# Kernel tuning notes

Measured on AMD Instinct MI355X. Metric: run time of the kernel, lower is better.

The kernel has to match this reference:

```python
import jax, jax.numpy as jnp
import numpy as np

B, N, F_IN, F_HID, F_OUT = 32, 1024, 512, 512, 512


def setup_inputs() -> dict:
    key = jax.random.key(0)
    ks = jax.random.split(key, 8)
    def xavier(k, fan_in, fan_out):
        bound = float(np.sqrt(6.0 / (fan_in + fan_out)))
        return jax.random.uniform(k, (fan_in, fan_out), jnp.float32, -bound, bound)
    return {
        "batch_graph": jax.random.normal(ks[0], (B, N, F_IN), jnp.float32),
        "adj": jax.random.uniform(ks[1], (B, N, N), jnp.float32),
        "W1": xavier(ks[2], F_IN, F_HID),
        "b1": jnp.zeros((F_HID,), jnp.float32),
        "W2": xavier(ks[3], F_HID, F_HID),
        "b2": jnp.zeros((F_HID,), jnp.float32),
        "W3": xavier(ks[4], F_HID, F_OUT),
        "b3": jnp.zeros((F_OUT,), jnp.float32),
    }


def _gcn_layer(x, adj, W, b):
    # support = X @ W ; out = A @ support + b  (per graph in the batch)
    support = jnp.einsum("bnf,fh->bnh", x, W)
    return jnp.einsum("bnm,bmh->bnh", adj, support) + b


def reference(batch_graph, adj, W1, b1, W2, b2, W3, b3):
    # Block-diagonal big_adj @ big_graph is exactly a batched per-graph matmul:
    # the zero off-diagonal blocks contribute nothing, so math is identical.
    # Dropout is identity at inference (eval mode).
    x = jax.nn.relu(_gcn_layer(batch_graph, adj, W1, b1))
    x = jax.nn.relu(_gcn_layer(x, adj, W2, b2))
    out = _gcn_layer(x, adj, W3, b3)  # [B, N, F_OUT]
    return out
```

## Files before the change

kernel.cpp:

```cpp
#include <hip/hip_runtime.h>
#include <hip/hip_bf16.h>


typedef __attribute__((ext_vector_type(8))) short bf16x8s;
typedef __attribute__((ext_vector_type(4))) float f32x4;
typedef __attribute__((ext_vector_type(4))) unsigned short us4;
typedef __attribute__((ext_vector_type(8))) unsigned short us8;

__device__ __forceinline__ unsigned short f2bf(float f) {
    unsigned u = __builtin_bit_cast(unsigned, f);
    u += 0x7fffu + ((u >> 16) & 1u);
    return (unsigned short)(u >> 16);
}

__device__ __forceinline__ us8 pack8(float4 a, float4 b) {
    us8 o;
    o[0] = f2bf(a.x); o[1] = f2bf(a.y); o[2] = f2bf(a.z); o[3] = f2bf(a.w);
    o[4] = f2bf(b.x); o[5] = f2bf(b.y); o[6] = f2bf(b.z); o[7] = f2bf(b.w);
    return o;
}

__device__ __forceinline__ void async16(const unsigned short* g, unsigned short* l) {
    __builtin_amdgcn_global_load_lds(
        (const __attribute__((address_space(1))) unsigned int*)g,
        (__attribute__((address_space(3))) unsigned int*)l, 16, 0, 0);
}

#define MFMA_(d, va, vb) d = __builtin_amdgcn_mfma_f32_16x16x32_bf16(va, vb, d, 0, 0, 0)

__global__ void prep(const float* __restrict__ W1, const float* __restrict__ W2,
                     const float* __restrict__ W3, unsigned short* __restrict__ WT1,
                     unsigned short* __restrict__ WT2, unsigned short* __restrict__ WT3) {
    constexpr int F = 512;
    const long FF = (long)F * F;
    const long S = (long)gridDim.x * 256;
    for (long k = (long)blockIdx.x * 256 + threadIdx.x; k < 3 * FF; k += S) {
        int w = (int)(k / FF);
        long idx = k % FF;
        int r = (int)(idx % F);
        int c = (int)(idx / F);
        const float* W = (w == 0) ? W1 : (w == 1) ? W2 : W3;
        unsigned short* WT = (w == 0) ? WT1 : (w == 1) ? WT2 : WT3;
        WT[idx] = f2bf(W[(size_t)r * F + c]);
    }
}

__global__ __launch_bounds__(512, 2)
void gemm_g1f(const unsigned short* __restrict__ WT,
              const float* __restrict__ X0,
              unsigned short* __restrict__ PT)
{
    constexpr int K = 512, NN = 1024;
    constexpr int nt = K >> 6;
    __shared__ unsigned short Lraw[65536];

    const int t = threadIdx.x, lane = t & 63, wv = t >> 6;
    const int wm = wv >> 2, wn = wv & 3;
    const int fr = lane & 15, fk = (lane >> 4) * 8, r4 = (lane >> 4) * 4;
    const int lb = ((int)blockIdx.x & 7) * 32 + ((int)blockIdx.x >> 3);
    const int bat = lb >> 3, tt = lb & 7;
    const int m0 = (tt >> 2) << 8, n0 = (tt & 3) << 8;

    const unsigned short* Ab = WT + (size_t)m0 * K;
    const float* Bb = X0 + (size_t)bat * NN * K + (size_t)n0 * K;

    int srow[2], scol[2], lo[2];
#pragma unroll
    for (int r = 0; r < 2; ++r) {
        int c   = r * 512 + t;
        srow[r] = c >> 3;
        scol[r] = ((c & 7) * 8) ^ ((srow[r] & 7) << 3);
        lo[r]   = c * 8;
    }

    auto stageA = [&](int kt, int h) {
        unsigned short* base = Lraw + (kt & 1) * 16384;
#pragma unroll
        for (int r = 0; r < 2; ++r)
            async16(Ab + (size_t)(h * 128 + srow[r]) * K + kt * 64 + scol[r],
                    base + h * 8192 + lo[r]);
    };
    auto rdA = [&](int buf, int mf, int kkj) -> bf16x8s {
        int row = wm * 128 + mf * 16 + fr;
        int e   = (kkj * 32 + fk) ^ ((row & 7) << 3);
        return *(const bf16x8s*)&Lraw[buf * 16384 + row * 64 + e];
    };
    auto rdB = [&](int buf, int nf, int kkj) -> bf16x8s {
        int row = wn * 64 + nf * 16 + fr;
        int e   = (kkj * 32 + fk) ^ ((row & 7) << 3);
        return *(const bf16x8s*)&Lraw[32768 + buf * 16384 + row * 64 + e];
    };

    float4 fa[4], fb[4];
    auto loadB = [&](int kt) {
#pragma unroll
        for (int h = 0; h < 2; ++h)
#pragma unroll
            for (int r = 0; r < 2; ++r) {
                const float* p = Bb + (size_t)(h * 128 + srow[r]) * K + kt * 64 + scol[r];
                fa[h * 2 + r] = *(const float4*)p;
                fb[h * 2 + r] = *(const float4*)(p + 4);
            }
    };
    auto writeB = [&](int buf) {
#pragma unroll
        for (int h = 0; h < 2; ++h)
#pragma unroll
            for (int r = 0; r < 2; ++r)
                *(us8*)&Lraw[32768 + buf * 16384 + h * 8192 + lo[r]] =
                    pack8(fa[h * 2 + r], fb[h * 2 + r]);
    };

    f32x4 acc[8][4];
#pragma unroll
    for (int i = 0; i < 8; ++i)
#pragma unroll
        for (int j = 0; j < 4; ++j) acc[i][j] = f32x4{0.f, 0.f, 0.f, 0.f};
    bf16x8s aP[4], aB[4], aC[4], bX[4], bY[4];

    loadB(0);
    stageA(0, 0); stageA(0, 1);
    writeB(0);
    loadB(1);
    asm volatile("s_waitcnt vmcnt(8)" ::: "memory");
    __syncthreads();
#pragma unroll
    for (int m = 0; m < 4; ++m) aP[m] = rdA(0, m, 0);
#pragma unroll
    for (int n = 0; n < 4; ++n) bX[n] = rdB(0, n, 0);

    for (int it = 0; it < nt; ++it) {
        const int cur = it & 1, nxt = cur ^ 1;
        const bool m1 = it + 1 < nt, m2 = it + 2 < nt;

        __builtin_amdgcn_s_barrier();
#pragma unroll
        for (int m = 0; m < 4; ++m) aB[m] = rdA(cur, m + 4, 0);
        if (m1) { stageA(it + 1, 0); stageA(it + 1, 1); }
        __builtin_amdgcn_s_setprio(1);
#pragma unroll
        for (int m = 0; m < 4; ++m)
#pragma unroll
            for (int n = 0; n < 4; ++n) MFMA_(acc[m][n], aP[m], bX[n]);
        __builtin_amdgcn_s_setprio(0);

        __builtin_amdgcn_s_barrier();
#pragma unroll
        for (int m = 0; m < 4; ++m) aC[m] = rdA(cur, m, 1);
#pragma unroll
        for (int n = 0; n < 4; ++n) bY[n] = rdB(cur, n, 1);
        __builtin_amdgcn_s_setprio(1);
#pragma unroll
        for (int m = 0; m < 4; ++m)
#pragma unroll
            for (int n = 0; n < 4; ++n) MFMA_(acc[m + 4][n], aB[m], bX[n]);
        __builtin_amdgcn_s_setprio(0);

        __builtin_amdgcn_s_barrier();
#pragma unroll
        for (int m = 0; m < 4; ++m) aB[m] = rdA(cur, m + 4, 1);
        if (m1) writeB(nxt);
        if (m2) loadB(it + 2);
        __builtin_amdgcn_s_setprio(1);
#pragma unroll
        for (int m = 0; m < 4; ++m)
#pragma unroll
            for (int n = 0; n < 4; ++n) MFMA_(acc[m][n], aC[m], bY[n]);
        __builtin_amdgcn_s_setprio(0);

        if (m1) {
            if (m2) asm volatile("s_waitcnt vmcnt(8) lgkmcnt(0)" ::: "memory");
            else    asm volatile("s_waitcnt vmcnt(0) lgkmcnt(0)" ::: "memory");
            __builtin_amdgcn_s_barrier();
#pragma unroll
            for (int m = 0; m < 4; ++m) aP[m] = rdA(nxt, m, 0);
#pragma unroll
            for (int n = 0; n < 4; ++n) bX[n] = rdB(nxt, n, 0);
        }
        __builtin_amdgcn_s_setprio(1);
#pragma unroll
        for (int m = 0; m < 4; ++m)
#pragma unroll
            for (int n = 0; n < 4; ++n) MFMA_(acc[m + 4][n], aB[m], bY[n]);
        __builtin_amdgcn_s_setprio(0);
    }

    __syncthreads();
    const int R0 = m0 + wm * 128;
    const int C0 = n0 + wn * 64;
    unsigned short* sl = Lraw + wv * 8192;
#pragma unroll
    for (int i = 0; i < 8; ++i)
#pragma unroll
        for (int j = 0; j < 4; ++j)
#pragma unroll
            for (int e = 0; e < 4; ++e) {
                const int row = i * 16 + r4 + e;
                const int col = j * 16 + fr;
                sl[row * 64 + (col ^ ((row & 7) << 3))] = f2bf(acc[i][j][e]);
            }
    unsigned short* Cb = PT + (size_t)bat * 512 * 1024;
#pragma unroll
    for (int rr = 0; rr < 16; ++rr) {
        const int row = rr * 8 + (lane >> 3);
        const int k8  = lane & 7;
        us8 v = *(const us8*)&sl[row * 64 + ((k8 ^ (row & 7)) << 3)];
        *(us8*)&Cb[(size_t)(R0 + row) * NN + C0 + k8 * 8] = v;
    }
}

__global__ __launch_bounds__(512, 2)
void gemm_g2f(const float* __restrict__ ADJ,
              unsigned short* __restrict__ adjb,
              const unsigned short* __restrict__ PT,
              unsigned short* __restrict__ P1,
              const float* __restrict__ bias)
{
    constexpr int K = 1024, NN = 512;
    constexpr int nt = K >> 6;
    __shared__ unsigned short Lraw[81920];

    const int t = threadIdx.x, lane = t & 63, wv = t >> 6;
    const int wm = wv >> 2, wn = wv & 3;
    const int fr = lane & 15, fk = (lane >> 4) * 8, r4 = (lane >> 4) * 4;
    const int lb = ((int)blockIdx.x & 7) * 32 + ((int)blockIdx.x >> 3);
    const int bat = lb >> 3, tt = lb & 7;
    const int m0 = (tt >> 1) << 8, n0 = (tt & 1) << 8;
    const bool wb = (n0 == 0);

    const float* Afb = ADJ + (size_t)bat * K * K + (size_t)m0 * K;
    unsigned short* Awb = adjb + (size_t)bat * K * K + (size_t)m0 * K;
    const unsigned short* Bb = PT + (size_t)bat * NN * K + (size_t)n0 * K;

    int srow[2], scol[2], lo[2];
#pragma unroll
    for (int r = 0; r < 2; ++r) {
        int c   = r * 512 + t;
        srow[r] = c >> 3;
        scol[r] = ((c & 7) * 8) ^ ((srow[r] & 7) << 3);
        lo[r]   = c * 8;
    }

    auto stageB = [&](int buf, int kt) {
        unsigned short* base = Lraw + 32768 + buf * 16384;
#pragma unroll
        for (int h = 0; h < 2; ++h)
#pragma unroll
            for (int r = 0; r < 2; ++r)
                async16(Bb + (size_t)(h * 128 + srow[r]) * K + kt * 64 + scol[r],
                        base + h * 8192 + lo[r]);
    };
    auto rdA = [&](int buf, int mf, int kkj) -> bf16x8s {
        int row = wm * 128 + mf * 16 + fr;
        int e   = (kkj * 32 + fk) ^ ((row & 7) << 3);
        return *(const bf16x8s*)&Lraw[buf * 16384 + row * 64 + e];
    };
    auto rdB = [&](int buf, int nf, int kkj) -> bf16x8s {
        int row = wn * 64 + nf * 16 + fr;
        int e   = (kkj * 32 + fk) ^ ((row & 7) << 3);
        return *(const bf16x8s*)&Lraw[32768 + buf * 16384 + row * 64 + e];
    };

    float4 fa[4], fb[4];
    auto loadA = [&](int kt) {
#pragma unroll
        for (int h = 0; h < 2; ++h)
#pragma unroll
            for (int r = 0; r < 2; ++r) {
                const float* p = Afb + (size_t)(h * 128 + srow[r]) * K + kt * 64 + scol[r];
                fa[h * 2 + r] = *(const float4*)p;
                fb[h * 2 + r] = *(const float4*)(p + 4);
            }
    };
    auto flushA = [&](int buf, int kt) {
#pragma unroll
        for (int h = 0; h < 2; ++h)
#pragma unroll
            for (int r = 0; r < 2; ++r) {
                us8 v = pack8(fa[h * 2 + r], fb[h * 2 + r]);
                *(us8*)&Lraw[buf * 16384 + h * 8192 + lo[r]] = v;
                if (wb)
                    *(us8*)&Awb[(size_t)(h * 128 + srow[r]) * K + kt * 64 + scol[r]] = v;
            }
    };

    f32x4 acc[8][4];
#pragma unroll
    for (int i = 0; i < 8; ++i)
#pragma unroll
        for (int j = 0; j < 4; ++j) acc[i][j] = f32x4{0.f, 0.f, 0.f, 0.f};
    bf16x8s aP[4], aB[4], aC[4], bX[4], bY[4];

    loadA(0);
    stageB(0, 0); stageB(1, 1);
    flushA(0, 0);
    loadA(1);
    asm volatile("s_waitcnt vmcnt(4)" ::: "memory");
    __syncthreads();
#pragma unroll
    for (int m = 0; m < 4; ++m) aP[m] = rdA(0, m, 0);
#pragma unroll
    for (int n = 0; n < 4; ++n) bX[n] = rdB(0, n, 0);

    int bc = 0;
    for (int it = 0; it < nt; ++it) {
        const int cur = it & 1, nxt = cur ^ 1;
        const int bn1 = (bc == 2) ? 0 : bc + 1;
        const int bn2 = (bn1 == 2) ? 0 : bn1 + 1;
        const bool m1 = it + 1 < nt, m2 = it + 2 < nt;

        __builtin_amdgcn_s_barrier();
#pragma unroll
        for (int m = 0; m < 4; ++m) aB[m] = rdA(cur, m + 4, 0);
        __builtin_amdgcn_s_setprio(1);
#pragma unroll
        for (int m = 0; m < 4; ++m)
#pragma unroll
            for (int n = 0; n < 4; ++n) MFMA_(acc[m][n], aP[m], bX[n]);
        __builtin_amdgcn_s_setprio(0);

        __builtin_amdgcn_s_barrier();
#pragma unroll
        for (int m = 0; m < 4; ++m) aC[m] = rdA(cur, m, 1);
#pragma unroll
        for (int n = 0; n < 4; ++n) bY[n] = rdB(bc, n, 1);
        __builtin_amdgcn_s_setprio(1);
#pragma unroll
        for (int m = 0; m < 4; ++m)
#pragma unroll
            for (int n = 0; n < 4; ++n) MFMA_(acc[m + 4][n], aB[m], bX[n]);
        __builtin_amdgcn_s_setprio(0);

        __builtin_amdgcn_s_barrier();
#pragma unroll
        for (int m = 0; m < 4; ++m) aB[m] = rdA(cur, m + 4, 1);
        if (m1) flushA(nxt, it + 1);
        if (m2) stageB(bn2, it + 2);
        __builtin_amdgcn_s_setprio(1);
#pragma unroll
        for (int m = 0; m < 4; ++m)
#pragma unroll
            for (int n = 0; n < 4; ++n) MFMA_(acc[m][n], aC[m], bY[n]);
        __builtin_amdgcn_s_setprio(0);

        if (m1) {
            if (m2) asm volatile("s_waitcnt vmcnt(12) lgkmcnt(0)" ::: "memory");
            else    asm volatile("s_waitcnt vmcnt(0) lgkmcnt(0)" ::: "memory");
            __builtin_amdgcn_s_barrier();
#pragma unroll
            for (int m = 0; m < 4; ++m) aP[m] = rdA(nxt, m, 0);
#pragma unroll
            for (int n = 0; n < 4; ++n) bX[n] = rdB(bn1, n, 0);
            if (m2) loadA(it + 2);
        }
        __builtin_amdgcn_s_setprio(1);
#pragma unroll
        for (int m = 0; m < 4; ++m)
#pragma unroll
            for (int n = 0; n < 4; ++n) MFMA_(acc[m + 4][n], aB[m], bY[n]);
        __builtin_amdgcn_s_setprio(0);
        bc = bn1;
    }

    __syncthreads();
    const int R0 = m0 + wm * 128;
    const int C0 = n0 + wn * 64;
    float bv[4];
#pragma unroll
    for (int j = 0; j < 4; ++j) bv[j] = bias[C0 + j * 16 + fr];
    unsigned short* sl = Lraw + wv * 8192;
#pragma unroll
    for (int i = 0; i < 8; ++i)
#pragma unroll
        for (int j = 0; j < 4; ++j)
#pragma unroll
            for (int e = 0; e < 4; ++e) {
                const int row = i * 16 + r4 + e;
                const int col = j * 16 + fr;
                sl[row * 64 + (col ^ ((row & 7) << 3))] =
                    f2bf(fmaxf(acc[i][j][e] + bv[j], 0.f));
            }
    unsigned short* Cb = P1 + (size_t)bat * 1024 * 512;
#pragma unroll
    for (int rr = 0; rr < 16; ++rr) {
        const int row = rr * 8 + (lane >> 3);
        const int k8  = lane & 7;
        us8 v = *(const us8*)&sl[row * 64 + ((k8 ^ (row & 7)) << 3)];
        *(us8*)&Cb[(size_t)(R0 + row) * NN + C0 + k8 * 8] = v;
    }
}

template<bool RELU, bool OUT_F32>
__global__ __launch_bounds__(512, 2)
void gemm256(const unsigned short* __restrict__ A,
             const unsigned short* __restrict__ BT,
             void* __restrict__ Cout,
             const float* __restrict__ bias,
             int M, int N, int K,
             long sA, long sBT, long sC)
{
    __shared__ unsigned short Lraw[81920];

    const int t    = threadIdx.x;
    const int lane = t & 63;
    const int wv   = t >> 6;
    const int wm   = wv >> 2;
    const int wn   = wv & 3;
    const int fr   = lane & 15;
    const int fk   = (lane >> 4) * 8;
    const int r4   = (lane >> 4) * 4;

    const int tilesN = N >> 8;
    const int bpb    = (M >> 8) * tilesN;
    const int cpx = gridDim.x >> 3;
    const int lb  = (blockIdx.x & 7) * cpx + (blockIdx.x >> 3);
    const int bat = lb / bpb;
    const int tt  = lb % bpb;
    const int m0  = (tt / tilesN) << 8;
    const int n0  = (tt % tilesN) << 8;

    const unsigned short* Ab = A  + (size_t)bat * sA  + (size_t)m0 * K;
    const unsigned short* Bb = BT + (size_t)bat * sBT + (size_t)n0 * K;

    int srow[2], scol[2], lo[2];
#pragma unroll
    for (int r = 0; r < 2; ++r) {
        int c   = r * 512 + t;
        srow[r] = c >> 3;
        scol[r] = ((c & 7) * 8) ^ ((srow[r] & 7) << 3);
        lo[r]   = c * 8;
    }

    auto stageA = [&](int kt, int h) {
        unsigned short* base = Lraw + (kt & 1) * 16384;
#pragma unroll
        for (int r = 0; r < 2; ++r)
            async16(Ab + (size_t)(h * 128 + srow[r]) * K + kt * 64 + scol[r],
                    base + h * 8192 + lo[r]);
    };
    auto stageB = [&](int buf, int kt) {
        unsigned short* base = Lraw + 32768 + buf * 16384;
#pragma unroll
        for (int h = 0; h < 2; ++h)
#pragma unroll
            for (int r = 0; r < 2; ++r)
                async16(Bb + (size_t)(h * 128 + srow[r]) * K + kt * 64 + scol[r],
                        base + h * 8192 + lo[r]);
    };
    auto rdA = [&](int buf, int mf, int kkj) -> bf16x8s {
        int row = wm * 128 + mf * 16 + fr;
        int e   = (kkj * 32 + fk) ^ ((row & 7) << 3);
        return *(const bf16x8s*)&Lraw[buf * 16384 + row * 64 + e];
    };
    auto rdB = [&](int buf, int nf, int kkj) -> bf16x8s {
        int row = wn * 64 + nf * 16 + fr;
        int e   = (kkj * 32 + fk) ^ ((row & 7) << 3);
        return *(const bf16x8s*)&Lraw[32768 + buf * 16384 + row * 64 + e];
    };

    const int nt = K >> 6;

    f32x4 acc[8][4];
#pragma unroll
    for (int i = 0; i < 8; ++i)
#pragma unroll
        for (int j = 0; j < 4; ++j) acc[i][j] = f32x4{0.f, 0.f, 0.f, 0.f};

    bf16x8s aP[4], aB[4], aC[4], bX[4], bY[4];

    stageA(0, 0); stageA(0, 1);
    stageB(0, 0);
    if (nt > 1) {
        stageB(1, 1);
        asm volatile("s_waitcnt vmcnt(4)" ::: "memory");
    } else {
        asm volatile("s_waitcnt vmcnt(0)" ::: "memory");
    }
    __builtin_amdgcn_s_barrier();
#pragma unroll
    for (int m = 0; m < 4; ++m) aP[m] = rdA(0, m, 0);
#pragma unroll
    for (int n = 0; n < 4; ++n) bX[n] = rdB(0, n, 0);

    int bc = 0;
    for (int it = 0; it < nt; ++it) {
        const int cur = it & 1;
        const int bn1 = (bc == 2) ? 0 : bc + 1;
        const int bn2 = (bn1 == 2) ? 0 : bn1 + 1;
        const bool m1 = (it + 1 < nt), m2 = (it + 2 < nt);

        __builtin_amdgcn_s_barrier();
#pragma unroll
        for (int m = 0; m < 4; ++m) aB[m] = rdA(cur, m + 4, 0);
        if (m1) stageA(it + 1, 0);
        __builtin_amdgcn_s_setprio(1);
#pragma unroll
        for (int m = 0; m < 4; ++m)
#pragma unroll
            for (int n = 0; n < 4; ++n) MFMA_(acc[m][n], aP[m], bX[n]);
        __builtin_amdgcn_s_setprio(0);

        __builtin_amdgcn_s_barrier();
#pragma unroll
        for (int m = 0; m < 4; ++m) aC[m] = rdA(cur, m, 1);
#pragma unroll
        for (int n = 0; n < 4; ++n) bY[n] = rdB(bc, n, 1);
        if (m1) stageA(it + 1, 1);
        __builtin_amdgcn_s_setprio(1);
#pragma unroll
        for (int m = 0; m < 4; ++m)
#pragma unroll
            for (int n = 0; n < 4; ++n) MFMA_(acc[m + 4][n], aB[m], bX[n]);
        __builtin_amdgcn_s_setprio(0);

        __builtin_amdgcn_s_barrier();
#pragma unroll
        for (int m = 0; m < 4; ++m) aB[m] = rdA(cur, m + 4, 1);
        if (m2) stageB(bn2, it + 2);
        __builtin_amdgcn_s_setprio(1);
#pragma unroll
        for (int m = 0; m < 4; ++m)
#pragma unroll
            for (int n = 0; n < 4; ++n) MFMA_(acc[m][n], aC[m], bY[n]);
        __builtin_amdgcn_s_setprio(0);

        if (m1) {
            if (m2) asm volatile("s_waitcnt vmcnt(4)" ::: "memory");
            else    asm volatile("s_waitcnt vmcnt(0)" ::: "memory");
            __builtin_amdgcn_s_barrier();
#pragma unroll
            for (int m = 0; m < 4; ++m) aP[m] = rdA(cur ^ 1, m, 0);
#pragma unroll
            for (int n = 0; n < 4; ++n) bX[n] = rdB(bn1, n, 0);
        }
        __builtin_amdgcn_s_setprio(1);
#pragma unroll
        for (int m = 0; m < 4; ++m)
#pragma unroll
            for (int n = 0; n < 4; ++n) MFMA_(acc[m + 4][n], aB[m], bY[n]);
        __builtin_amdgcn_s_setprio(0);
        bc = bn1;
    }

    __syncthreads();

    const int R0 = m0 + wm * 128;
    const int C0 = n0 + wn * 64;
    float bv[4];
#pragma unroll
    for (int j = 0; j < 4; ++j)
        bv[j] = bias ? bias[C0 + j * 16 + fr] : 0.f;

    if (OUT_F32) {
        float* Cb = (float*)Cout + (size_t)bat * sC;
#pragma unroll
        for (int j = 0; j < 4; ++j)
#pragma unroll
            for (int i = 0; i < 8; ++i)
#pragma unroll
                for (int e = 0; e < 4; ++e) {
                    float v = acc[i][j][e] + bv[j];
                    if (RELU) v = fmaxf(v, 0.f);
                    Cb[(size_t)(R0 + i * 16 + r4 + e) * N + C0 + j * 16 + fr] = v;
                }
    } else {
        unsigned short* sl = Lraw + wv * 8192;
#pragma unroll
        for (int i = 0; i < 8; ++i)
#pragma unroll
            for (int j = 0; j < 4; ++j)
#pragma unroll
                for (int e = 0; e < 4; ++e) {
                    float v = acc[i][j][e] + bv[j];
                    if (RELU) v = fmaxf(v, 0.f);
                    const int row = i * 16 + r4 + e;
                    const int col = j * 16 + fr;
                    sl[row * 64 + (col ^ ((row & 7) << 3))] = f2bf(v);
                }
        unsigned short* Cb = (unsigned short*)Cout + (size_t)bat * sC;
#pragma unroll
        for (int rr = 0; rr < 16; ++rr) {
            const int row = rr * 8 + (lane >> 3);
            const int k8  = lane & 7;
            us8 v = *(const us8*)&sl[row * 64 + ((k8 ^ (row & 7)) << 3)];
            *(us8*)&Cb[(size_t)(R0 + row) * N + C0 + k8 * 8] = v;
        }
    }
}

extern "C" void kernel_launch(void* const* d_in, const int* in_sizes, int n_in,
                              void* d_out, int out_size, void* d_ws, size_t ws_size,
                              hipStream_t stream) {
    constexpr int B = 32, N = 1024, F = 512;

    const float* x0f  = (const float*)d_in[0];
    const float* adjf = (const float*)d_in[1];
    const float* W1 = (const float*)d_in[2];
    const float* b1 = (const float*)d_in[3];
    const float* W2 = (const float*)d_in[4];
    const float* b2 = (const float*)d_in[5];
    const float* W3 = (const float*)d_in[6];
    const float* b3 = (const float*)d_in[7];

    unsigned short* ws   = (unsigned short*)d_ws;
    unsigned short* adjb = ws;
    unsigned short* P0   = adjb + (size_t)B * N * N;
    unsigned short* P1   = P0 + (size_t)B * N * F;
    unsigned short* PT   = P1 + (size_t)B * N * F;
    unsigned short* WT1  = PT + (size_t)B * N * F;
    unsigned short* WT2  = WT1 + (size_t)F * F;
    unsigned short* WT3  = WT2 + (size_t)F * F;

    prep<<<256, 256, 0, stream>>>(W1, W2, W3, WT1, WT2, WT3);

    const int grid = 256;
    const long sX = (long)N * F;
    const long sAd = (long)N * N;

    gemm_g1f<<<grid, 512, 0, stream>>>(WT1, x0f, PT);
    gemm_g2f<<<grid, 512, 0, stream>>>(adjf, adjb, PT, P1, b1);
    gemm256<false, false><<<grid, 512, 0, stream>>>(WT2,  P1, PT, nullptr, F, N, F, 0,  sX, sX);
    gemm256<true,  false><<<grid, 512, 0, stream>>>(adjb, PT, P0, b2,      N, F, N, sAd, sX, sX);
    gemm256<false, false><<<grid, 512, 0, stream>>>(WT3,  P0, PT, nullptr, F, N, F, 0,  sX, sX);
    gemm256<false, true ><<<grid, 512, 0, stream>>>(adjb, PT, (float*)d_out, b3, N, F, N, sAd, sX, sX);
}
```

Before: 231.5 us.

## Stage fp32 adjacency tiles into LDS asynchronously and convert to bf16 on read

The first-layer adjacency GEMM now copies fp32 adj tiles straight into double-buffered LDS with async global-to-LDS loads, instead of loading them through registers and packing them to bf16 before the LDS store. Conversion to bf16 moves to LDS read time, using the packed v_cvt_pk_bf16_f32 instruction. The bf16 copy of adj is written back to global memory from the LDS tile. The B operand drops to a single buffer. The goal is to take the global-load latency and the conversion arithmetic off the register path and overlap them with MFMA work. In exchange, A reads from LDS double in bytes, every wave repeats the conversion for shared rows, and B has less prefetch depth.

```diff
diff --git a/kernel.cpp b/kernel.cpp
--- a/kernel.cpp
+++ b/kernel.cpp
@@ -18,6 +18,21 @@
     o[0] = f2bf(a.x); o[1] = f2bf(a.y); o[2] = f2bf(a.z); o[3] = f2bf(a.w);
     o[4] = f2bf(b.x); o[5] = f2bf(b.y); o[6] = f2bf(b.z); o[7] = f2bf(b.w);
     return o;
+}
+
+__device__ __forceinline__ bf16x8s cvt8(float4 a, float4 b) {
+    int4 r;
+    asm("v_cvt_pk_bf16_f32 %0, %1, %2" : "=v"(r.x) : "v"(a.x), "v"(a.y));
+    asm("v_cvt_pk_bf16_f32 %0, %1, %2" : "=v"(r.y) : "v"(a.z), "v"(a.w));
+    asm("v_cvt_pk_bf16_f32 %0, %1, %2" : "=v"(r.z) : "v"(b.x), "v"(b.y));
+    asm("v_cvt_pk_bf16_f32 %0, %1, %2" : "=v"(r.w) : "v"(b.z), "v"(b.w));
+    return __builtin_bit_cast(bf16x8s, r);
+}
+__device__ __forceinline__ us4 cvt4(float4 a) {
+    int2 r;
+    asm("v_cvt_pk_bf16_f32 %0, %1, %2" : "=v"(r.x) : "v"(a.x), "v"(a.y));
+    asm("v_cvt_pk_bf16_f32 %0, %1, %2" : "=v"(r.y) : "v"(a.z), "v"(a.w));
+    return __builtin_bit_cast(us4, r);
 }
 
 __device__ __forceinline__ void async16(const unsigned short* g, unsigned short* l) {
@@ -218,7 +233,8 @@
 {
     constexpr int K = 1024, NN = 512;
     constexpr int nt = K >> 6;
-    __shared__ unsigned short Lraw[81920];
+    __shared__ float Af[2][16384];
+    __shared__ unsigned short Bl[16384];
 
     const int t = threadIdx.x, lane = t & 63, wv = t >> 6;
     const int wm = wv >> 2, wn = wv & 3;
@@ -240,48 +256,47 @@
         scol[r] = ((c & 7) * 8) ^ ((srow[r] & 7) << 3);
         lo[r]   = c * 8;
     }
-
-    auto stageB = [&](int buf, int kt) {
-        unsigned short* base = Lraw + 32768 + buf * 16384;
+    auto stageB = [&](int kt) {
 #pragma unroll
         for (int h = 0; h < 2; ++h)
 #pragma unroll
             for (int r = 0; r < 2; ++r)
                 async16(Bb + (size_t)(h * 128 + srow[r]) * K + kt * 64 + scol[r],
-                        base + h * 8192 + lo[r]);
-    };
-    auto rdA = [&](int buf, int mf, int kkj) -> bf16x8s {
-        int row = wm * 128 + mf * 16 + fr;
-        int e   = (kkj * 32 + fk) ^ ((row & 7) << 3);
-        return *(const bf16x8s*)&Lraw[buf * 16384 + row * 64 + e];
-    };
-    auto rdB = [&](int buf, int nf, int kkj) -> bf16x8s {
+                        Bl + h * 8192 + lo[r]);
+    };
+    auto rdB = [&](int nf, int kkj) -> bf16x8s {
         int row = wn * 64 + nf * 16 + fr;
         int e   = (kkj * 32 + fk) ^ ((row & 7) << 3);
-        return *(const bf16x8s*)&Lraw[32768 + buf * 16384 + row * 64 + e];
-    };
-
-    float4 fa[4], fb[4];
-    auto loadA = [&](int kt) {
-#pragma unroll
-        for (int h = 0; h < 2; ++h)
-#pragma unroll
-            for (int r = 0; r < 2; ++r) {
-                const float* p = Afb + (size_t)(h * 128 + srow[r]) * K + kt * 64 + scol[r];
-                fa[h * 2 + r] = *(const float4*)p;
-                fb[h * 2 + r] = *(const float4*)(p + 4);
-            }
-    };
-    auto flushA = [&](int buf, int kt) {
-#pragma unroll
-        for (int h = 0; h < 2; ++h)
-#pragma unroll
-            for (int r = 0; r < 2; ++r) {
-                us8 v = pack8(fa[h * 2 + r], fb[h * 2 + r]);
-                *(us8*)&Lraw[buf * 16384 + h * 8192 + lo[r]] = v;
-                if (wb)
-                    *(us8*)&Awb[(size_t)(h * 128 + srow[r]) * K + kt * 64 + scol[r]] = v;
-            }
+        return *(const bf16x8s*)&Bl[row * 64 + e];
+    };
+
+    auto stageAf = [&](int kt, int half) {
+#pragma unroll
+        for (int q = half * 4; q < half * 4 + 4; ++q) {
+            int c   = q * 512 + t;
+            int row = c >> 4;
+            int us  = (c & 15) ^ (row & 15);
+            async16((const unsigned short*)(Afb + (size_t)row * K + kt * 64 + us * 4),
+                    (unsigned short*)&Af[kt & 1][(size_t)c * 4]);
+        }
+    };
+    auto rdAf = [&](int buf, int mf, int kkj) -> bf16x8s {
+        int row = wm * 128 + mf * 16 + fr;
+        int u   = (kkj * 32 + fk) >> 2;
+        int r15 = row & 15;
+        float4 a = *(const float4*)&Af[buf][row * 64 + ((u ^ r15) << 2)];
+        float4 b = *(const float4*)&Af[buf][row * 64 + (((u + 1) ^ r15) << 2)];
+        return cvt8(a, b);
+    };
+    auto wbTile = [&](int buf, int kt) {
+#pragma unroll
+        for (int q = 0; q < 8; ++q) {
+            int c   = q * 512 + t;
+            int row = c >> 4;
+            int us  = (c & 15) ^ (row & 15);
+            float4 v = *(const float4*)&Af[buf][(size_t)c * 4];
+            *(us4*)&Awb[(size_t)row * K + kt * 64 + us * 4] = cvt4(v);
+        }
     };
 
     f32x4 acc[8][4];
@@ -291,27 +306,25 @@
         for (int j = 0; j < 4; ++j) acc[i][j] = f32x4{0.f, 0.f, 0.f, 0.f};
     bf16x8s aP[4], aB[4], aC[4], bX[4], bY[4];
 
-    loadA(0);
-    stageB(0, 0); stageB(1, 1);
-    flushA(0, 0);
-    loadA(1);
-    asm volatile("s_waitcnt vmcnt(4)" ::: "memory");
+    stageAf(0, 0); stageAf(0, 1);
+    stageB(0);
+    asm volatile("s_waitcnt vmcnt(0)" ::: "memory");
     __syncthreads();
 #pragma unroll
-    for (int m = 0; m < 4; ++m) aP[m] = rdA(0, m, 0);
-#pragma unroll
-    for (int n = 0; n < 4; ++n) bX[n] = rdB(0, n, 0);
-
-    int bc = 0;
+    for (int m = 0; m < 4; ++m) aP[m] = rdAf(0, m, 0);
+#pragma unroll
+    for (int n = 0; n < 4; ++n) bX[n] = rdB(n, 0);
+
     for (int it = 0; it < nt; ++it) {
         const int cur = it & 1, nxt = cur ^ 1;
-        const int bn1 = (bc == 2) ? 0 : bc + 1;
-        const int bn2 = (bn1 == 2) ? 0 : bn1 + 1;
-        const bool m1 = it + 1 < nt, m2 = it + 2 < nt;
-
-        __builtin_amdgcn_s_barrier();
-#pragma unroll
-        for (int m = 0; m < 4; ++m) aB[m] = rdA(cur, m + 4, 0);
+        const bool m1 = it + 1 < nt;
+
+        __builtin_amdgcn_s_barrier();
+#pragma unroll
+        for (int m = 0; m < 4; ++m) aB[m] = rdAf(cur, m + 4, 0);
+#pragma unroll
+        for (int n = 0; n < 4; ++n) bY[n] = rdB(n, 1);
+        if (m1) stageAf(it + 1, 0);
         __builtin_amdgcn_s_setprio(1);
 #pragma unroll
         for (int m = 0; m < 4; ++m)
@@ -321,9 +334,8 @@
 
         __builtin_amdgcn_s_barrier();
 #pragma unroll
-        for (int m = 0; m < 4; ++m) aC[m] = rdA(cur, m, 1);
-#pragma unroll
-        for (int n = 0; n < 4; ++n) bY[n] = rdB(bc, n, 1);
+        for (int m = 0; m < 4; ++m) aC[m] = rdAf(cur, m, 1);
+        if (m1) { stageAf(it + 1, 1); stageB(it + 1); }
         __builtin_amdgcn_s_setprio(1);
 #pragma unroll
         for (int m = 0; m < 4; ++m)
@@ -333,9 +345,8 @@
 
         __builtin_amdgcn_s_barrier();
 #pragma unroll
-        for (int m = 0; m < 4; ++m) aB[m] = rdA(cur, m + 4, 1);
-        if (m1) flushA(nxt, it + 1);
-        if (m2) stageB(bn2, it + 2);
+        for (int m = 0; m < 4; ++m) aB[m] = rdAf(cur, m + 4, 1);
+        if (wb) wbTile(cur, it);
         __builtin_amdgcn_s_setprio(1);
 #pragma unroll
         for (int m = 0; m < 4; ++m)
@@ -344,14 +355,13 @@
         __builtin_amdgcn_s_setprio(0);
 
         if (m1) {
-            if (m2) asm volatile("s_waitcnt vmcnt(12) lgkmcnt(0)" ::: "memory");
-            else    asm volatile("s_waitcnt vmcnt(0) lgkmcnt(0)" ::: "memory");
+            if (wb) asm volatile("s_waitcnt vmcnt(8)" ::: "memory");
+            else    asm volatile("s_waitcnt vmcnt(0)" ::: "memory");
             __builtin_amdgcn_s_barrier();
 #pragma unroll
-            for (int m = 0; m < 4; ++m) aP[m] = rdA(nxt, m, 0);
-#pragma unroll
-            for (int n = 0; n < 4; ++n) bX[n] = rdB(bn1, n, 0);
-            if (m2) loadA(it + 2);
+            for (int m = 0; m < 4; ++m) aP[m] = rdAf(nxt, m, 0);
+#pragma unroll
+            for (int n = 0; n < 4; ++n) bX[n] = rdB(n, 0);
         }
         __builtin_amdgcn_s_setprio(1);
 #pragma unroll
@@ -359,7 +369,6 @@
 #pragma unroll
             for (int n = 0; n < 4; ++n) MFMA_(acc[m + 4][n], aB[m], bY[n]);
         __builtin_amdgcn_s_setprio(0);
-        bc = bn1;
     }
 
     __syncthreads();
@@ -368,7 +377,7 @@
     float bv[4];
 #pragma unroll
     for (int j = 0; j < 4; ++j) bv[j] = bias[C0 + j * 16 + fr];
-    unsigned short* sl = Lraw + wv * 8192;
+    unsigned short* sl = (unsigned short*)Af + wv * 8192;
 #pragma unroll
     for (int i = 0; i < 8; ++i)
 #pragma unroll
@@ -380,6 +389,7 @@
                 sl[row * 64 + (col ^ ((row & 7) << 3))] =
                     f2bf(fmaxf(acc[i][j][e] + bv[j], 0.f));
             }
+    __syncthreads();
     unsigned short* Cb = P1 + (size_t)bat * 1024 * 512;
 #pragma unroll
     for (int rr = 0; rr < 16; ++rr) {
```

Result: slower. 260.3 us (+12.4%).
